# Performance work log

Measured on AMD Instinct MI355X. Metric: run time of the kernel, lower is better.

The kernel has to match this reference:

```python
import jax, jax.numpy as jnp
import numpy as np

N = 100000   # active voxels (stride=1 -> output coords == input coords)
C_IN = 64
C_OUT = 64
K3 = 27      # 3x3x3 kernel offsets
M = 40000    # rulebook pairs per kernel offset
EPS = 1e-5


def setup_inputs() -> dict:
    key = jax.random.key(0)
    k1, k2, k3, k4 = jax.random.split(key, 4)
    x = jax.random.normal(k1, (N, C_IN), dtype=jnp.float32)
    # conv weights per kernel offset: [K3, inc, outc]
    W = jax.random.normal(k2, (K3, C_IN, C_OUT), dtype=jnp.float32) * 0.05
    gamma = jnp.ones((C_OUT,), dtype=jnp.float32)
    beta = jnp.zeros((C_OUT,), dtype=jnp.float32)
    # rulebook: for each offset k, M (input_idx, output_idx) pairs
    in_idx = jax.random.randint(k3, (K3, M), 0, N, dtype=jnp.int32)
    out_idx = jax.random.randint(k4, (K3, M), 0, N, dtype=jnp.int32)
    return {"x": x, "W": W, "gamma": gamma, "beta": beta,
            "in_idx": in_idx, "out_idx": out_idx}


def reference(x, W, gamma, beta, in_idx, out_idx):
    n_out = x.shape[0]  # stride=1: output voxel set == input voxel set
    # gather: [K3, M, C_IN]
    feat = x[in_idx]
    # batched GEMM over kernel offsets: [K3, M, C_OUT]
    contrib = jnp.einsum('kmi,kio->kmo', feat, W)
    # scatter-add into output voxels
    out = jnp.zeros((n_out, W.shape[2]), dtype=x.dtype)
    out = out.at[out_idx.reshape(-1)].add(contrib.reshape(-1, W.shape[2]))
    # BatchNorm over active points (training-mode batch stats, biased var)
    mean = jnp.mean(out, axis=0)
    var = jnp.mean(jnp.square(out - mean), axis=0)
    y = (out - mean) * jax.lax.rsqrt(var + EPS) * gamma + beta
    # ReLU
    return jnp.maximum(y, 0.0)
```

## Files before the change

kernel.cpp:

```cpp
#include <hip/hip_runtime.h>


#define N_VOX   100000
#define NPAD    100096
#define K3      27
#define M_PAIRS 40000
#define NPAIRS  (K3 * M_PAIRS)
#define BN_EPS  1e-5f
#define NBINS   (K3 * NPAD)
#define AUXMAX  49152
#define AUXCAP  (AUXMAX - 1)
#define ZROW    (N_VOX + AUXMAX - 1)

#define OFF_WT     0u
#define OFF_STATS  221184u
#define OFF_CTRS   221696u
#define OFF_BG2    221760u
#define OFF_NODE   21842496u
#define OFF_LIST   30482496u
#define OFF_XB     30679104u
#define OFF_BH     49770560u

#define NB_WT    432
#define NB_XB    3125
#define NB_BUILD 4219
#define GRID_IB  (NB_WT + NB_XB + 1 + NB_BUILD)

typedef __attribute__((ext_vector_type(8))) short bf16x8;
typedef __attribute__((ext_vector_type(4))) float f32x4;

__device__ __forceinline__ short f2bf(float f) {
  unsigned u = __builtin_bit_cast(unsigned, f);
  u += 0x7FFFu + ((u >> 16) & 1u);
  return (short)(u >> 16);
}
__device__ __forceinline__ float bf2f(short s) {
  unsigned u = ((unsigned)(unsigned short)s) << 16;
  return __builtin_bit_cast(float, u);
}

__global__ __launch_bounds__(256) void init_build_kernel(const float* __restrict__ W,
                                                         const float* __restrict__ x,
                                                         const int* __restrict__ in_idx,
                                                         const int* __restrict__ out_idx,
                                                         short* __restrict__ wt,
                                                         short* __restrict__ xb,
                                                         int* __restrict__ bh,
                                                         int2* __restrict__ node) {
  int b = blockIdx.x, t = threadIdx.x;
  if (b < NB_WT) {
    int id = b * 256 + t;
    int k = id >> 12, rem = id & 4095, c = rem >> 6, i = rem & 63;
    wt[id] = f2bf(W[(k << 12) + (i << 6) + c]);
  } else if (b < NB_WT + NB_XB) {
    int id = (b - NB_WT) * 256 + t;
    if (id < N_VOX * 8) {
      float4 lo = ((const float4*)x)[id * 2];
      float4 hi = ((const float4*)x)[id * 2 + 1];
      bf16x8 v;
      v[0] = f2bf(lo.x); v[1] = f2bf(lo.y); v[2] = f2bf(lo.z); v[3] = f2bf(lo.w);
      v[4] = f2bf(hi.x); v[5] = f2bf(hi.y); v[6] = f2bf(hi.z); v[7] = f2bf(hi.w);
      ((bf16x8*)xb)[id] = v;
    }
  } else if (b == NB_WT + NB_XB) {
    if (t < 8) {
      bf16x8 z = {0, 0, 0, 0, 0, 0, 0, 0};
      ((bf16x8*)(xb + (size_t)ZROW * 64))[t] = z;
    }
  } else {
    int id = (b - (NB_WT + NB_XB + 1)) * 256 + t;
    if (id < NPAIRS) {
      int k  = id / M_PAIRS;
      int in = in_idx[id];
      int o  = out_idx[id];
      int bb = k * NPAD + o;
      int old = atomicExch(&bh[bb], id);
      node[id] = make_int2(old, in);
    }
  }
}

__global__ __launch_bounds__(256) void compact_kernel(const int* __restrict__ bh,
                                                      const int2* __restrict__ node,
                                                      int2* __restrict__ bg2,
                                                      int* __restrict__ list,
                                                      int* __restrict__ ctrs) {
  __shared__ int l_cnt, l_base;
  int t = threadIdx.x;
  if (t == 0) l_cnt = 0;
  __syncthreads();
  int w = blockIdx.x * 256 + t;
  bool ok = (w < NBINS / 4);
  int4 h4 = ok ? ((const int4*)bh)[w] : make_int4(-1, -1, -1, -1);
  int hv[4] = {h4.x, h4.y, h4.z, h4.w};
  int g0[4], g1[4], lp[4];
  #pragma unroll
  for (int s = 0; s < 4; ++s) {
    lp[s] = -1; g0[s] = ZROW; g1[s] = ZROW;
    if (hv[s] >= 0) {
      int2 n0 = node[hv[s]];
      g0[s] = n0.y;
      if (n0.x >= 0) {
        int2 n1 = node[n0.x];
        g1[s] = n1.y;
        if (n1.x >= 0) lp[s] = atomicAdd(&l_cnt, 1);
      }
    }
  }
  __syncthreads();
  if (t == 0) l_base = (l_cnt > 0) ? atomicAdd(&ctrs[0], l_cnt) : 0;
  __syncthreads();
  #pragma unroll
  for (int s = 0; s < 4; ++s) {
    if (lp[s] >= 0) {
      int pos = l_base + lp[s];
      if (pos < AUXCAP) { list[pos] = hv[s]; g0[s] = N_VOX + pos; g1[s] = ZROW; }
    }
  }
  if (ok) {
    ((int4*)bg2)[w * 2]     = make_int4(g0[0], g1[0], g0[1], g1[1]);
    ((int4*)bg2)[w * 2 + 1] = make_int4(g0[2], g1[2], g0[3], g1[3]);
  }
}

__global__ __launch_bounds__(256) void fixup_kernel(short* __restrict__ xb,
                                                    const int* __restrict__ list,
                                                    const int2* __restrict__ node,
                                                    const int* __restrict__ ctrs) {
  int n = ctrs[0]; if (n > AUXCAP) n = AUXCAP;
  int wid  = (blockIdx.x * 256 + threadIdx.x) >> 6;
  int lane = threadIdx.x & 63;
  int nw   = gridDim.x * 4;
  for (int i = wid; i < n; i += nw) {
    int h = list[i];
    float acc = 0.f;
    while (h >= 0) {
      int2 nd = node[h];
      acc += bf2f(xb[(size_t)nd.y * 64 + lane]);
      h = nd.x;
    }
    xb[(size_t)(N_VOX + i) * 64 + lane] = f2bf(acc);
  }
}

#define LOADROW(d0, d1, idx)                                    \
  { const short* _p = xb + (size_t)(idx) * 64;                  \
    d0 = *(const bf16x8*)(_p + g8);                             \
    d1 = *(const bf16x8*)(_p + 32 + g8); }

__global__ __launch_bounds__(256) void conv_out_kernel(const short* __restrict__ xb,
                                                       const short* __restrict__ wt,
                                                       const int2* __restrict__ bg,
                                                       float* __restrict__ out,
                                                       float* __restrict__ stats) {
  __shared__ short lds[2 * 4096];
  __shared__ float ls[128];
  int t = threadIdx.x, wave = t >> 6, lane = t & 63;
  int g = lane >> 4, c0 = lane & 15, g8 = g * 8;
  int o0 = blockIdx.x * 128 + wave * 32 + c0;
  int o1 = o0 + 16;

  int rb  = ((c0 * 128 + g * 16) ^ ((c0 & 7) << 4)) >> 1;
  int wb0 = ((t * 32) ^ (((t >> 2) & 7) << 4)) >> 1;
  if (t < 128) ls[t] = 0.f;

  f32x4 acc0[4], acc1[4];
  #pragma unroll
  for (int n = 0; n < 4; ++n) {
    acc0[n][0]=0.f; acc0[n][1]=0.f; acc0[n][2]=0.f; acc0[n][3]=0.f;
    acc1[n][0]=0.f; acc1[n][1]=0.f; acc1[n][2]=0.f; acc1[n][3]=0.f;
  }

  bf16x8 s0w = *(const bf16x8*)(wt + t * 16);
  bf16x8 s1w = *(const bf16x8*)(wt + t * 16 + 8);
  int2 gac = bg[o0], gbc = bg[o1];
  bf16x8 ap0c, ap1c, as0c, as1c, bp0c, bp1c, bs0c, bs1c;
  LOADROW(ap0c, ap1c, gac.x); LOADROW(as0c, as1c, gac.y);
  LOADROW(bp0c, bp1c, gbc.x); LOADROW(bs0c, bs1c, gbc.y);
  int2 gan = bg[NPAD + o0], gbn = bg[NPAD + o1];
  *(bf16x8*)&lds[wb0]     = s0w;
  *(bf16x8*)&lds[wb0 ^ 8] = s1w;
  __syncthreads();

  int buf = 0;
  for (int k = 0; k < K3; ++k) {
    if (k + 1 < K3) {
      const short* wn = wt + (size_t)(k + 1) * 4096 + t * 16;
      s0w = *(const bf16x8*)(wn);
      s1w = *(const bf16x8*)(wn + 8);
    }
    bf16x8 ap0n, ap1n, as0n, as1n, bp0n, bp1n, bs0n, bs1n;
    LOADROW(ap0n, ap1n, gan.x); LOADROW(as0n, as1n, gan.y);
    LOADROW(bp0n, bp1n, gbn.x); LOADROW(bs0n, bs1n, gbn.y);
    int2 gann = make_int2(ZROW, ZROW), gbnn = make_int2(ZROW, ZROW);
    if (k + 2 < K3) {
      gann = bg[(size_t)(k + 2) * NPAD + o0];
      gbnn = bg[(size_t)(k + 2) * NPAD + o1];
    }
    const short* lb = lds + buf * 4096;
    #pragma unroll
    for (int n = 0; n < 4; ++n) {
      bf16x8 b0 = *(const bf16x8*)&lb[rb + n * 1024];
      bf16x8 b1 = *(const bf16x8*)&lb[(rb ^ 32) + n * 1024];
      acc0[n] = __builtin_amdgcn_mfma_f32_16x16x32_bf16(ap0c, b0, acc0[n], 0, 0, 0);
      acc0[n] = __builtin_amdgcn_mfma_f32_16x16x32_bf16(ap1c, b1, acc0[n], 0, 0, 0);
      acc0[n] = __builtin_amdgcn_mfma_f32_16x16x32_bf16(as0c, b0, acc0[n], 0, 0, 0);
      acc0[n] = __builtin_amdgcn_mfma_f32_16x16x32_bf16(as1c, b1, acc0[n], 0, 0, 0);
      acc1[n] = __builtin_amdgcn_mfma_f32_16x16x32_bf16(bp0c, b0, acc1[n], 0, 0, 0);
      acc1[n] = __builtin_amdgcn_mfma_f32_16x16x32_bf16(bp1c, b1, acc1[n], 0, 0, 0);
      acc1[n] = __builtin_amdgcn_mfma_f32_16x16x32_bf16(bs0c, b0, acc1[n], 0, 0, 0);
      acc1[n] = __builtin_amdgcn_mfma_f32_16x16x32_bf16(bs1c, b1, acc1[n], 0, 0, 0);
    }
    if (k + 1 < K3) {
      short* wd = lds + (buf ^ 1) * 4096;
      *(bf16x8*)&wd[wb0]     = s0w;
      *(bf16x8*)&wd[wb0 ^ 8] = s1w;
    }
    __syncthreads();
    ap0c = ap0n; ap1c = ap1n; as0c = as0n; as1c = as1n;
    bp0c = bp0n; bp1c = bp1n; bs0c = bs0n; bs1c = bs1n;
    gan = gann; gbn = gbnn; buf ^= 1;
  }

  int orow = blockIdx.x * 128 + wave * 32 + (g << 2);
  #pragma unroll
  for (int j = 0; j < 4; ++j) {
    int r0 = orow + j, r1 = orow + 16 + j;
    if (r0 < N_VOX) {
      float* op = out + (size_t)r0 * 64 + c0;
      op[0] = acc0[0][j]; op[16] = acc0[1][j]; op[32] = acc0[2][j]; op[48] = acc0[3][j];
    }
    if (r1 < N_VOX) {
      float* op = out + (size_t)r1 * 64 + c0;
      op[0] = acc1[0][j]; op[16] = acc1[1][j]; op[32] = acc1[2][j]; op[48] = acc1[3][j];
    }
  }

  #pragma unroll
  for (int n = 0; n < 4; ++n) {
    float s = 0.f, q = 0.f;
    #pragma unroll
    for (int j = 0; j < 4; ++j) {
      float v0 = acc0[n][j], v1 = acc1[n][j];
      s += v0 + v1; q += v0 * v0 + v1 * v1;
    }
    atomicAdd(&ls[n * 16 + c0], s);
    atomicAdd(&ls[64 + n * 16 + c0], q);
  }
  __syncthreads();
  if (t < 128) unsafeAtomicAdd(&stats[t], ls[t]);
}

__global__ __launch_bounds__(256) void norm_kernel(float* __restrict__ out,
                                                   const float* __restrict__ stats,
                                                   const float* __restrict__ gamma,
                                                   const float* __restrict__ beta) {
  int i4 = blockIdx.x * 256 + threadIdx.x;
  if (i4 >= N_VOX * 16) return;
  const float invN = 1.0f / (float)N_VOX;
  float4 v = ((const float4*)out)[i4];
  int c0 = (i4 << 2) & 63;
  float r[4] = {v.x, v.y, v.z, v.w};
  #pragma unroll
  for (int j = 0; j < 4; ++j) {
    int c = c0 + j;
    float mean = stats[c] * invN;
    float ex2  = stats[64 + c] * invN;
    float var  = ex2 - mean * mean;
    float scale = gamma[c] * rsqrtf(var + BN_EPS);
    float shift = beta[c] - mean * scale;
    r[j] = fmaxf(r[j] * scale + shift, 0.0f);
  }
  v.x = r[0]; v.y = r[1]; v.z = r[2]; v.w = r[3];
  ((float4*)out)[i4] = v;
}

extern "C" void kernel_launch(void* const* d_in, const int* in_sizes, int n_in,
                              void* d_out, int out_size, void* d_ws, size_t ws_size,
                              hipStream_t stream) {
  const float* x      = (const float*)d_in[0];
  const float* W      = (const float*)d_in[1];
  const float* gamma  = (const float*)d_in[2];
  const float* beta   = (const float*)d_in[3];
  const int*   in_idx = (const int*)d_in[4];
  const int*   out_idx= (const int*)d_in[5];
  float* out = (float*)d_out;

  char* ws = (char*)d_ws;
  short* wt    = (short*)(ws + OFF_WT);
  float* stats = (float*)(ws + OFF_STATS);
  int*   ctrs  = (int*)(ws + OFF_CTRS);
  int2*  bg2   = (int2*)(ws + OFF_BG2);
  int2*  node  = (int2*)(ws + OFF_NODE);
  int*   list  = (int*)(ws + OFF_LIST);
  short* xb    = (short*)(ws + OFF_XB);
  int*   bh    = (int*)(ws + OFF_BH);

  hipMemsetAsync(ws + OFF_STATS, 0, OFF_BG2 - OFF_STATS, stream);
  hipMemsetAsync((void*)bh, 0xFF, (size_t)NBINS * 4, stream);

  init_build_kernel<<<GRID_IB, 256, 0, stream>>>(W, x, in_idx, out_idx,
                                                 wt, xb, bh, node);
  compact_kernel<<<(NBINS / 4 + 255) / 256, 256, 0, stream>>>(bh, node, bg2, list, ctrs);
  fixup_kernel<<<1024, 256, 0, stream>>>(xb, list, node, ctrs);
  conv_out_kernel<<<NPAD / 128, 256, 0, stream>>>(xb, wt, bg2, out, stats);
  norm_kernel<<<(N_VOX * 16 + 255) / 256, 256, 0, stream>>>(out, stats, gamma, beta);
}
```

Before: 216.3 us.

## Pack bin heads as 64-bit with multi-flag, single gather slot per output

Bin heads now hold the input index and pair id in one 64-bit word, plus a flag set when a bin collides. The compact kernel no longer chases node pointers. Any bin with more than one pair is pre-summed into an auxiliary row, so each (offset, output) needs only one gathered row instead of two, which halves MFMA work and gather loads in the conv kernel. The cost is more pre-summed rows in the fixup pass, 64-bit atomics and memset, and a larger aux buffer. The fixup grid is also doubled.

```diff
diff --git a/kernel.cpp b/kernel.cpp
--- a/kernel.cpp
+++ b/kernel.cpp
@@ -8,18 +8,21 @@
 #define NPAIRS  (K3 * M_PAIRS)
 #define BN_EPS  1e-5f
 #define NBINS   (K3 * NPAD)
-#define AUXMAX  49152
+#define AUXMAX  184320
 #define AUXCAP  (AUXMAX - 1)
 #define ZROW    (N_VOX + AUXMAX - 1)
+#define SENT    0xFFFFFFFFFFFFFFFFull
+#define MFLAG   (1ull << 63)
 
 #define OFF_WT     0u
 #define OFF_STATS  221184u
 #define OFF_CTRS   221696u
-#define OFF_BG2    221760u
-#define OFF_NODE   21842496u
-#define OFF_LIST   30482496u
-#define OFF_XB     30679104u
-#define OFF_BH     49770560u
+#define OFF_GINX   221760u
+#define OFF_NODE   11032128u
+#define OFF_LIST   19672128u
+#define OFF_XB     21146688u
+#define OFF_BH     (OFF_XB + 12800000u)
+#define WS_NEED    ((size_t)OFF_XB + (size_t)(N_VOX + AUXMAX) * 128u)
 
 #define NB_WT    432
 #define NB_XB    3125
@@ -28,6 +31,7 @@
 
 typedef __attribute__((ext_vector_type(8))) short bf16x8;
 typedef __attribute__((ext_vector_type(4))) float f32x4;
+typedef unsigned long long u64;
 
 __device__ __forceinline__ short f2bf(float f) {
   unsigned u = __builtin_bit_cast(unsigned, f);
@@ -45,8 +49,8 @@
                                                          const int* __restrict__ out_idx,
                                                          short* __restrict__ wt,
                                                          short* __restrict__ xb,
-                                                         int* __restrict__ bh,
-                                                         int2* __restrict__ node) {
+                                                         u64* __restrict__ bh,
+                                                         u64* __restrict__ node) {
   int b = blockIdx.x, t = threadIdx.x;
   if (b < NB_WT) {
     int id = b * 256 + t;
@@ -74,16 +78,17 @@
       int in = in_idx[id];
       int o  = out_idx[id];
       int bb = k * NPAD + o;
-      int old = atomicExch(&bh[bb], id);
-      node[id] = make_int2(old, in);
-    }
-  }
-}
-
-__global__ __launch_bounds__(256) void compact_kernel(const int* __restrict__ bh,
-                                                      const int2* __restrict__ node,
-                                                      int2* __restrict__ bg2,
-                                                      int* __restrict__ list,
+      u64 nh  = ((u64)(unsigned)in << 32) | (unsigned)id;
+      u64 old = atomicExch(&bh[bb], nh);
+      node[id] = old;
+      if (old != SENT) atomicOr(&bh[bb], MFLAG);
+    }
+  }
+}
+
+__global__ __launch_bounds__(256) void compact_kernel(const u64* __restrict__ bh,
+                                                      int* __restrict__ ginx,
+                                                      u64* __restrict__ list,
                                                       int* __restrict__ ctrs) {
   __shared__ int l_cnt, l_base;
   int t = threadIdx.x;
@@ -91,21 +96,21 @@
   __syncthreads();
   int w = blockIdx.x * 256 + t;
   bool ok = (w < NBINS / 4);
-  int4 h4 = ok ? ((const int4*)bh)[w] : make_int4(-1, -1, -1, -1);
-  int hv[4] = {h4.x, h4.y, h4.z, h4.w};
-  int g0[4], g1[4], lp[4];
+  u64 h[4];
+  if (ok) {
+    ulonglong2 p0 = ((const ulonglong2*)bh)[w * 2];
+    ulonglong2 p1 = ((const ulonglong2*)bh)[w * 2 + 1];
+    h[0] = p0.x; h[1] = p0.y; h[2] = p1.x; h[3] = p1.y;
+  } else {
+    h[0] = SENT; h[1] = SENT; h[2] = SENT; h[3] = SENT;
+  }
+  int gv[4], lp[4];
   #pragma unroll
   for (int s = 0; s < 4; ++s) {
-    lp[s] = -1; g0[s] = ZROW; g1[s] = ZROW;
-    if (hv[s] >= 0) {
-      int2 n0 = node[hv[s]];
-      g0[s] = n0.y;
-      if (n0.x >= 0) {
-        int2 n1 = node[n0.x];
-        g1[s] = n1.y;
-        if (n1.x >= 0) lp[s] = atomicAdd(&l_cnt, 1);
-      }
-    }
+    lp[s] = -1;
+    if (h[s] == SENT)            gv[s] = ZROW;
+    else if (!(h[s] >> 63))      gv[s] = (int)((h[s] >> 32) & 0x7FFFFFFFu);
+    else                         lp[s] = atomicAdd(&l_cnt, 1);
   }
   __syncthreads();
   if (t == 0) l_base = (l_cnt > 0) ? atomicAdd(&ctrs[0], l_cnt) : 0;
@@ -114,43 +119,40 @@
   for (int s = 0; s < 4; ++s) {
     if (lp[s] >= 0) {
       int pos = l_base + lp[s];
-      if (pos < AUXCAP) { list[pos] = hv[s]; g0[s] = N_VOX + pos; g1[s] = ZROW; }
-    }
-  }
-  if (ok) {
-    ((int4*)bg2)[w * 2]     = make_int4(g0[0], g1[0], g0[1], g1[1]);
-    ((int4*)bg2)[w * 2 + 1] = make_int4(g0[2], g1[2], g0[3], g1[3]);
-  }
+      if (pos < AUXCAP) { list[pos] = h[s]; gv[s] = N_VOX + pos; }
+      else              { gv[s] = (int)((h[s] >> 32) & 0x7FFFFFFFu); }
+    }
+  }
+  if (ok) ((int4*)ginx)[w] = make_int4(gv[0], gv[1], gv[2], gv[3]);
 }
 
 __global__ __launch_bounds__(256) void fixup_kernel(short* __restrict__ xb,
-                                                    const int* __restrict__ list,
-                                                    const int2* __restrict__ node,
+                                                    const u64* __restrict__ list,
+                                                    const u64* __restrict__ node,
                                                     const int* __restrict__ ctrs) {
   int n = ctrs[0]; if (n > AUXCAP) n = AUXCAP;
   int wid  = (blockIdx.x * 256 + threadIdx.x) >> 6;
   int lane = threadIdx.x & 63;
   int nw   = gridDim.x * 4;
   for (int i = wid; i < n; i += nw) {
-    int h = list[i];
-    float acc = 0.f;
-    while (h >= 0) {
-      int2 nd = node[h];
-      acc += bf2f(xb[(size_t)nd.y * 64 + lane]);
-      h = nd.x;
+    u64 h = list[i];
+    int in0     = (int)((h >> 32) & 0x7FFFFFFFu);
+    unsigned id = (unsigned)(h & 0xFFFFFFFFu);
+    float acc = bf2f(xb[(size_t)in0 * 64 + lane]);
+    u64 v = node[id];
+    while (v != SENT) {
+      int in = (int)((v >> 32) & 0x7FFFFFFFu);
+      id = (unsigned)(v & 0xFFFFFFFFu);
+      acc += bf2f(xb[(size_t)in * 64 + lane]);
+      v = node[id];
     }
     xb[(size_t)(N_VOX + i) * 64 + lane] = f2bf(acc);
   }
 }
-
-#define LOADROW(d0, d1, idx)                                    \
-  { const short* _p = xb + (size_t)(idx) * 64;                  \
-    d0 = *(const bf16x8*)(_p + g8);                             \
-    d1 = *(const bf16x8*)(_p + 32 + g8); }
 
 __global__ __launch_bounds__(256) void conv_out_kernel(const short* __restrict__ xb,
                                                        const short* __restrict__ wt,
-                                                       const int2* __restrict__ bg,
+                                                       const int* __restrict__ ginx,
                                                        float* __restrict__ out,
                                                        float* __restrict__ stats) {
   __shared__ short lds[2 * 4096];
@@ -173,11 +175,14 @@
 
   bf16x8 s0w = *(const bf16x8*)(wt + t * 16);
   bf16x8 s1w = *(const bf16x8*)(wt + t * 16 + 8);
-  int2 gac = bg[o0], gbc = bg[o1];
-  bf16x8 ap0c, ap1c, as0c, as1c, bp0c, bp1c, bs0c, bs1c;
-  LOADROW(ap0c, ap1c, gac.x); LOADROW(as0c, as1c, gac.y);
-  LOADROW(bp0c, bp1c, gbc.x); LOADROW(bs0c, bs1c, gbc.y);
-  int2 gan = bg[NPAD + o0], gbn = bg[NPAD + o1];
+  int ia = ginx[o0], ib = ginx[o1];
+  const short* xa = xb + (size_t)ia * 64;
+  const short* xc = xb + (size_t)ib * 64;
+  bf16x8 a0c = *(const bf16x8*)(xa + g8);
+  bf16x8 a1c = *(const bf16x8*)(xa + 32 + g8);
+  bf16x8 a2c = *(const bf16x8*)(xc + g8);
+  bf16x8 a3c = *(const bf16x8*)(xc + 32 + g8);
+  int i1a = ginx[NPAD + o0], i1b = ginx[NPAD + o1];
   *(bf16x8*)&lds[wb0]     = s0w;
   *(bf16x8*)&lds[wb0 ^ 8] = s1w;
   __syncthreads();
@@ -189,27 +194,26 @@
       s0w = *(const bf16x8*)(wn);
       s1w = *(const bf16x8*)(wn + 8);
     }
-    bf16x8 ap0n, ap1n, as0n, as1n, bp0n, bp1n, bs0n, bs1n;
-    LOADROW(ap0n, ap1n, gan.x); LOADROW(as0n, as1n, gan.y);
-    LOADROW(bp0n, bp1n, gbn.x); LOADROW(bs0n, bs1n, gbn.y);
-    int2 gann = make_int2(ZROW, ZROW), gbnn = make_int2(ZROW, ZROW);
+    const short* pa = xb + (size_t)i1a * 64;
+    const short* pb = xb + (size_t)i1b * 64;
+    bf16x8 a0n = *(const bf16x8*)(pa + g8);
+    bf16x8 a1n = *(const bf16x8*)(pa + 32 + g8);
+    bf16x8 a2n = *(const bf16x8*)(pb + g8);
+    bf16x8 a3n = *(const bf16x8*)(pb + 32 + g8);
+    int i2a = ZROW, i2b = ZROW;
     if (k + 2 < K3) {
-      gann = bg[(size_t)(k + 2) * NPAD + o0];
-      gbnn = bg[(size_t)(k + 2) * NPAD + o1];
+      i2a = ginx[(size_t)(k + 2) * NPAD + o0];
+      i2b = ginx[(size_t)(k + 2) * NPAD + o1];
     }
     const short* lb = lds + buf * 4096;
     #pragma unroll
     for (int n = 0; n < 4; ++n) {
       bf16x8 b0 = *(const bf16x8*)&lb[rb + n * 1024];
       bf16x8 b1 = *(const bf16x8*)&lb[(rb ^ 32) + n * 1024];
-      acc0[n] = __builtin_amdgcn_mfma_f32_16x16x32_bf16(ap0c, b0, acc0[n], 0, 0, 0);
-      acc0[n] = __builtin_amdgcn_mfma_f32_16x16x32_bf16(ap1c, b1, acc0[n], 0, 0, 0);
-      acc0[n] = __builtin_amdgcn_mfma_f32_16x16x32_bf16(as0c, b0, acc0[n], 0, 0, 0);
-      acc0[n] = __builtin_amdgcn_mfma_f32_16x16x32_bf16(as1c, b1, acc0[n], 0, 0, 0);
-      acc1[n] = __builtin_amdgcn_mfma_f32_16x16x32_bf16(bp0c, b0, acc1[n], 0, 0, 0);
-      acc1[n] = __builtin_amdgcn_mfma_f32_16x16x32_bf16(bp1c, b1, acc1[n], 0, 0, 0);
-      acc1[n] = __builtin_amdgcn_mfma_f32_16x16x32_bf16(bs0c, b0, acc1[n], 0, 0, 0);
-      acc1[n] = __builtin_amdgcn_mfma_f32_16x16x32_bf16(bs1c, b1, acc1[n], 0, 0, 0);
+      acc0[n] = __builtin_amdgcn_mfma_f32_16x16x32_bf16(a0c, b0, acc0[n], 0, 0, 0);
+      acc0[n] = __builtin_amdgcn_mfma_f32_16x16x32_bf16(a1c, b1, acc0[n], 0, 0, 0);
+      acc1[n] = __builtin_amdgcn_mfma_f32_16x16x32_bf16(a2c, b0, acc1[n], 0, 0, 0);
+      acc1[n] = __builtin_amdgcn_mfma_f32_16x16x32_bf16(a3c, b1, acc1[n], 0, 0, 0);
     }
     if (k + 1 < K3) {
       short* wd = lds + (buf ^ 1) * 4096;
@@ -217,9 +221,8 @@
       *(bf16x8*)&wd[wb0 ^ 8] = s1w;
     }
     __syncthreads();
-    ap0c = ap0n; ap1c = ap1n; as0c = as0n; as1c = as1n;
-    bp0c = bp0n; bp1c = bp1n; bs0c = bs0n; bs1c = bs1n;
-    gan = gann; gbn = gbnn; buf ^= 1;
+    a0c = a0n; a1c = a1n; a2c = a2n; a3c = a3n;
+    i1a = i2a; i1b = i2b; buf ^= 1;
   }
 
   int orow = blockIdx.x * 128 + wave * 32 + (g << 2);
@@ -290,19 +293,19 @@
   short* wt    = (short*)(ws + OFF_WT);
   float* stats = (float*)(ws + OFF_STATS);
   int*   ctrs  = (int*)(ws + OFF_CTRS);
-  int2*  bg2   = (int2*)(ws + OFF_BG2);
-  int2*  node  = (int2*)(ws + OFF_NODE);
-  int*   list  = (int*)(ws + OFF_LIST);
+  int*   ginx  = (int*)(ws + OFF_GINX);
+  u64*   node  = (u64*)(ws + OFF_NODE);
+  u64*   list  = (u64*)(ws + OFF_LIST);
   short* xb    = (short*)(ws + OFF_XB);
-  int*   bh    = (int*)(ws + OFF_BH);
-
-  hipMemsetAsync(ws + OFF_STATS, 0, OFF_BG2 - OFF_STATS, stream);
-  hipMemsetAsync((void*)bh, 0xFF, (size_t)NBINS * 4, stream);
+  u64*   bh    = (u64*)(ws + OFF_BH);
+
+  hipMemsetAsync(ws + OFF_STATS, 0, OFF_GINX - OFF_STATS, stream);
+  hipMemsetAsync((void*)bh, 0xFF, (size_t)NBINS * 8, stream);
 
   init_build_kernel<<<GRID_IB, 256, 0, stream>>>(W, x, in_idx, out_idx,
                                                  wt, xb, bh, node);
-  compact_kernel<<<(NBINS / 4 + 255) / 256, 256, 0, stream>>>(bh, node, bg2, list, ctrs);
-  fixup_kernel<<<1024, 256, 0, stream>>>(xb, list, node, ctrs);
-  conv_out_kernel<<<NPAD / 128, 256, 0, stream>>>(xb, wt, bg2, out, stats);
+  compact_kernel<<<(NBINS / 4 + 255) / 256, 256, 0, stream>>>(bh, ginx, list, ctrs);
+  fixup_kernel<<<2048, 256, 0, stream>>>(xb, list, node, ctrs);
+  conv_out_kernel<<<NPAD / 128, 256, 0, stream>>>(xb, wt, ginx, out, stats);
   norm_kernel<<<(N_VOX * 16 + 255) / 256, 256, 0, stream>>>(out, stats, gamma, beta);
 }
```

Result: slower. 235.9 us (+9.1%).
